# Performance work log

Hardware: AMD Instinct MI355X
Metric: run time of the kernel (lower is better)

## Reference

```python
import jax, jax.numpy as jnp
import numpy as np

B, T, D_IN, H, NUM_CLASSES = 512, 1024, 4, 64, 1098


def setup_inputs() -> dict:
    key = jax.random.key(0)
    ks = jax.random.split(key, 20)
    s = 1.0 / np.sqrt(H)  # PyTorch LSTM init range

    def w(k, shape):
        return jax.random.uniform(k, shape, jnp.float32, -s, s)

    inp = {}
    inp['x'] = jax.random.normal(ks[0], (B, T, D_IN), jnp.float32)
    lens = jax.random.randint(ks[1], (B,), 1, T + 1)
    inp['lengths'] = jnp.sort(lens)[::-1]  # descending, like pack_sequence
    i = 2
    for layer, d in ((0, D_IN), (1, 2 * H)):
        for dirn in ('f', 'b'):
            inp[f'W_ih_l{layer}{dirn}'] = w(ks[i], (4 * H, d)); i += 1
            inp[f'W_hh_l{layer}{dirn}'] = w(ks[i], (4 * H, H)); i += 1
            inp[f'b_ih_l{layer}{dirn}'] = w(ks[i], (4 * H,)); i += 1
            inp[f'b_hh_l{layer}{dirn}'] = w(ks[i], (4 * H,)); i += 1
    inp['W_out'] = w(ks[i], (NUM_CLASSES, 2 * H)); i += 1
    inp['b_out'] = w(ks[i], (NUM_CLASSES,))
    return inp


def _lstm_layer(x, W_ih, W_hh, b_ih, b_hh):
    # x: [B, T, D] -> outputs [B, T, H]; PyTorch gate order i, f, g, o
    Bb = x.shape[0]
    Hh = W_hh.shape[1]
    xW = jnp.einsum('btd,gd->btg', x, W_ih) + b_ih + b_hh  # [B, T, 4H]

    def step(carry, xt):
        h, c = carry
        g = xt + h @ W_hh.T
        i, f, gg, o = jnp.split(g, 4, axis=-1)
        c = jax.nn.sigmoid(f) * c + jax.nn.sigmoid(i) * jnp.tanh(gg)
        h = jax.nn.sigmoid(o) * jnp.tanh(c)
        return (h, c), h

    init = (jnp.zeros((Bb, Hh), x.dtype), jnp.zeros((Bb, Hh), x.dtype))
    _, hs = jax.lax.scan(step, init, jnp.swapaxes(xW, 0, 1))
    return jnp.swapaxes(hs, 0, 1)


def _reverse_padded(x, lengths):
    # per-sequence time reversal within the valid length (packed-seq semantics)
    Tt = x.shape[1]
    t = jnp.arange(Tt)
    idx = jnp.where(t[None, :] < lengths[:, None], lengths[:, None] - 1 - t[None, :], t[None, :])
    return jnp.take_along_axis(x, idx[:, :, None], axis=1)


def _bidir_layer(x, lengths, pf, pb):
    hf = _lstm_layer(x, *pf)
    hb = _reverse_padded(_lstm_layer(_reverse_padded(x, lengths), *pb), lengths)
    return jnp.concatenate([hf, hb], axis=-1)


def reference(x, lengths,
              W_ih_l0f, W_hh_l0f, b_ih_l0f, b_hh_l0f,
              W_ih_l0b, W_hh_l0b, b_ih_l0b, b_hh_l0b,
              W_ih_l1f, W_hh_l1f, b_ih_l1f, b_hh_l1f,
              W_ih_l1b, W_hh_l1b, b_ih_l1b, b_hh_l1b,
              W_out, b_out):
    h = _bidir_layer(x, lengths,
                     (W_ih_l0f, W_hh_l0f, b_ih_l0f, b_hh_l0f),
                     (W_ih_l0b, W_hh_l0b, b_ih_l0b, b_hh_l0b))
    h = _bidir_layer(h, lengths,
                     (W_ih_l1f, W_hh_l1f, b_ih_l1f, b_hh_l1f),
                     (W_ih_l1b, W_hh_l1b, b_ih_l1b, b_hh_l1b))
    # gather last valid timestep per sequence: [B, 2H]
    lasts = jnp.take_along_axis(h, (lengths - 1)[:, None, None], axis=1)[:, 0]
    return lasts @ W_out.T + b_out
```

## Files before the change

kernel.cpp:

```cpp
#include <hip/hip_runtime.h>
#include <stdint.h>

#define BATCH 512
#define TMAX  1024
#define DIN   4
#define H     64
#define NC    1098
#define RCH   32

typedef __attribute__((ext_vector_type(2))) float    v2;
typedef __attribute__((ext_vector_type(2))) _Float16 h2;

__device__ __forceinline__ v2 mkv2(float a, float b) { v2 r; r.x = a; r.y = b; return r; }
__device__ __forceinline__ float sigmoidf_(float x) { return 1.0f / (1.0f + __expf(-x)); }
__device__ __forceinline__ float tanhf_(float x) { return 1.0f - 2.0f / (__expf(2.0f * x) + 1.0f); }
__device__ __forceinline__ uint32_t f2bf(float f) {
    uint32_t u = __float_as_uint(f);
    return (u + 0x7FFFu + ((u >> 16) & 1u)) >> 16;
}
__device__ __forceinline__ float bf2f(uint32_t h) { return __uint_as_float(h << 16); }
__device__ __forceinline__ h2 u2h(uint32_t u) { union { uint32_t u; h2 h; } c; c.u = u; return c.h; }

__device__ __forceinline__ float fdot2_(h2 w, h2 x, float acc) {
    return __builtin_amdgcn_fdot2(w, x, acc, false);
}

__global__ __launch_bounds__(128) void lstm_l0(
    const float* __restrict__ x, const int* __restrict__ lengths,
    const float* __restrict__ Wih_f, const float* __restrict__ Whh_f,
    const float* __restrict__ bih_f, const float* __restrict__ bhh_f,
    const float* __restrict__ Wih_b, const float* __restrict__ Whh_b,
    const float* __restrict__ bih_b, const float* __restrict__ bhh_b,
    uint16_t* __restrict__ h0b )
{
    const int b = blockIdx.x;
    const int t = threadIdx.x;
    const int j = t & 63, dir = t >> 6;
    const int L = lengths[b];

    const float* Wih = dir ? Wih_b : Wih_f;
    const float* Whh = dir ? Whh_b : Whh_f;
    const float* bih = dir ? bih_b : bih_f;
    const float* bhh = dir ? bhh_b : bhh_f;

    h2 wh[4][32];
    #pragma unroll
    for (int g = 0; g < 4; g++) {
        const float4* pw = (const float4*)(Whh + (size_t)(64*g + j) * H);
        #pragma unroll
        for (int k = 0; k < 16; k++) {
            float4 a = pw[k];
            h2 lo; lo.x = (_Float16)a.x; lo.y = (_Float16)a.y;
            h2 hi; hi.x = (_Float16)a.z; hi.y = (_Float16)a.w;
            wh[g][2*k]   = lo;
            wh[g][2*k+1] = hi;
        }
    }
    float4 wx[4]; float bb[4];
    #pragma unroll
    for (int g = 0; g < 4; g++) {
        wx[g] = ((const float4*)Wih)[64*g + j];
        bb[g] = bih[64*g + j] + bhh[64*g + j];
    }

    __shared__ __align__(16) float4    xbuf[TMAX];
    __shared__ __align__(16) _Float16  hb16[2][H];
    {
        const float4* x4 = (const float4*)x + (size_t)b * TMAX;
        for (int i = t; i < L; i += 128) xbuf[i] = x4[i];
    }
    hb16[dir][j] = (_Float16)0.0f;
    float c = 0.0f;
    __syncthreads();

    uint16_t* outp = h0b + (size_t)b * TMAX * (2*H) + dir * H + j;

    for (int s = 0; s < L; s++) {
        const int tt = dir ? (L - 1 - s) : s;
        const float4 xt = xbuf[tt];
        float p[4];
        #pragma unroll
        for (int g = 0; g < 4; g++)
            p[g] = fmaf(wx[g].w, xt.w, fmaf(wx[g].z, xt.z,
                   fmaf(wx[g].y, xt.y, fmaf(wx[g].x, xt.x, bb[g]))));
        float acA[4] = {0.f,0.f,0.f,0.f}, acB[4] = {0.f,0.f,0.f,0.f};
        const uint4* h4 = (const uint4*)&hb16[dir][0];
        #pragma unroll
        for (int q = 0; q < 8; q++) {
            uint4 u = h4[q];
            h2 p0 = u2h(u.x), p1 = u2h(u.y), p2 = u2h(u.z), p3 = u2h(u.w);
            #pragma unroll
            for (int g = 0; g < 4; g++) {
                acA[g] = fdot2_(wh[g][4*q+0], p0, acA[g]);
                acA[g] = fdot2_(wh[g][4*q+1], p1, acA[g]);
                acB[g] = fdot2_(wh[g][4*q+2], p2, acB[g]);
                acB[g] = fdot2_(wh[g][4*q+3], p3, acB[g]);
            }
        }
        #pragma unroll
        for (int g = 0; g < 4; g++) p[g] += acA[g] + acB[g];
        const float gi = sigmoidf_(p[0]);
        const float gf = sigmoidf_(p[1]);
        const float gg = tanhf_(p[2]);
        const float go = sigmoidf_(p[3]);
        c = fmaf(gf, c, gi * gg);
        const float h = go * tanhf_(c);
        hb16[dir][j] = (_Float16)h;
        outp[(size_t)tt * (2*H)] = (uint16_t)f2bf(h);
    }
}

__global__ __launch_bounds__(512) void lstm_rec_pipe(
    const uint16_t* __restrict__ h0b, const int* __restrict__ lengths,
    const float* __restrict__ Wih, const float* __restrict__ Whh,
    const float* __restrict__ bih, const float* __restrict__ bhh,
    const float* __restrict__ Wih_b,
    const float* __restrict__ bih_b, const float* __restrict__ bhh_b,
    const float* __restrict__ Wout, const float* __restrict__ bout,
    float* __restrict__ out)
{
    const int b = blockIdx.x;
    const int t = threadIdx.x;
    const int j = t & 63, w = t >> 6;
    const int L = lengths[b];
    const bool isProd = (w < 4);

    __shared__ __align__(16) float xch[RCH * 128];
    __shared__ __align__(16) float part[2][4][256];
    __shared__ __align__(16) float hrep[4][H];
    __shared__ __align__(16) float ex[2][4][H];
    __shared__ __align__(16) float ybuf[2*H];

    v2 wreg[64];
    float bias = 0.0f;
    if (isProd) {
        #pragma unroll
        for (int q = 0; q < 4; q++) {
            const float4* pw = (const float4*)(Wih + (size_t)(4*j + q) * 128 + 32 * w);
            #pragma unroll
            for (int k = 0; k < 8; k++) {
                float4 v = pw[k];
                wreg[q*16 + 2*k]     = mkv2(v.x, v.y);
                wreg[q*16 + 2*k + 1] = mkv2(v.z, v.w);
            }
        }
    } else {
        const int g = (w - 4) * H + j;
        const float4* pw = (const float4*)(Whh + (size_t)g * H);
        #pragma unroll
        for (int k = 0; k < 16; k++) {
            float4 v = pw[k];
            wreg[2*k]     = mkv2(v.x, v.y);
            wreg[2*k + 1] = mkv2(v.z, v.w);
        }
        bias = bih[g] + bhh[g];
        hrep[w - 4][j] = 0.0f;
    }
    float c = 0.0f, h = 0.0f;

    auto produce = [&](int r, int p) {
        const float4* xr = (const float4*)(xch + r * 128 + 32 * w);
        v2 a0 = mkv2(0,0), a1 = mkv2(0,0), a2 = mkv2(0,0), a3 = mkv2(0,0);
        #pragma unroll
        for (int k = 0; k < 8; k++) {
            float4 xv = xr[k];
            v2 xlo = mkv2(xv.x, xv.y), xhi = mkv2(xv.z, xv.w);
            a0 += wreg[ 0 + 2*k] * xlo; a0 += wreg[ 0 + 2*k + 1] * xhi;
            a1 += wreg[16 + 2*k] * xlo; a1 += wreg[16 + 2*k + 1] * xhi;
            a2 += wreg[32 + 2*k] * xlo; a2 += wreg[32 + 2*k + 1] * xhi;
            a3 += wreg[48 + 2*k] * xlo; a3 += wreg[48 + 2*k + 1] * xhi;
        }
        *(float4*)&part[p][w][4*j] =
            make_float4(a0.x + a0.y, a1.x + a1.y, a2.x + a2.y, a3.x + a3.y);
    };

    for (int s = 0; s < L; s++) {
        const int rr = s & (RCH - 1);
        if (rr == 0) {
            __syncthreads();
            const uint32_t* src = (const uint32_t*)(h0b + ((size_t)b * TMAX + s) * (2*H));
            for (int i = t; i < RCH * 64; i += 512) {
                uint32_t u = src[i];
                *(float2*)(xch + 2*i) = make_float2(bf2f(u & 0xFFFFu), bf2f(u >> 16));
            }
            __syncthreads();
            if (isProd) produce(0, s & 1);
            __syncthreads();
        }
        if (isProd) {
            if (s + 1 < L && rr + 1 < RCH)
                produce(rr + 1, (s + 1) & 1);
        } else {
            const int g = (w - 4) * H + j;
            const float pa = part[s & 1][0][g] + part[s & 1][1][g]
                           + part[s & 1][2][g] + part[s & 1][3][g];
            v2 a0 = mkv2(pa + bias, 0.0f), a1 = mkv2(0.0f, 0.0f);
            const float4* h4 = (const float4*)hrep[w - 4];
            #pragma unroll
            for (int k = 0; k < 16; k++) {
                float4 hv = h4[k];
                a0 += wreg[2*k]     * mkv2(hv.x, hv.y);
                a1 += wreg[2*k + 1] * mkv2(hv.z, hv.w);
            }
            const float a = (a0.x + a0.y) + (a1.x + a1.y);
            ex[s & 1][w - 4][j] = (w == 6) ? tanhf_(a) : sigmoidf_(a);
        }
        __syncthreads();
        if (!isProd) {
            const int p = s & 1;
            const float gi = ex[p][0][j], gf = ex[p][1][j];
            const float gg = ex[p][2][j], go = ex[p][3][j];
            c = fmaf(gf, c, gi * gg);
            h = go * tanhf_(c);
            hrep[w - 4][j] = h;
        }
    }

    if (w == 4) ybuf[j] = h;
    __syncthreads();
    const float* xrow = xch + ((L - 1) & (RCH - 1)) * 128;
    float* gb = &part[0][0][0];
    if (t < 256) {
        const float4* wb = (const float4*)(Wih_b + (size_t)t * 128);
        const float4* xv = (const float4*)xrow;
        v2 a0 = mkv2(bih_b[t] + bhh_b[t], 0.0f), a1 = mkv2(0.0f, 0.0f);
        #pragma unroll
        for (int k = 0; k < 32; k++) {
            float4 wv = wb[k], xk = xv[k];
            a0 += mkv2(wv.x, wv.y) * mkv2(xk.x, xk.y);
            a1 += mkv2(wv.z, wv.w) * mkv2(xk.z, xk.w);
        }
        const float a = (a0.x + a0.y) + (a1.x + a1.y);
        gb[t] = (t >= 128 && t < 192) ? tanhf_(a) : sigmoidf_(a);
    }
    __syncthreads();
    if (t < 64) {
        const float gi = gb[t], gg = gb[128 + t], go = gb[192 + t];
        ybuf[H + t] = go * tanhf_(gi * gg);
    }
    __syncthreads();

    const float4* yv = (const float4*)ybuf;
    for (int o = t; o < NC; o += 512) {
        const float4* wr = (const float4*)(Wout + (size_t)o * (2*H));
        v2 a0 = mkv2(bout[o], 0.0f), a1 = mkv2(0.0f, 0.0f);
        #pragma unroll
        for (int k = 0; k < 32; k++) {
            float4 wv = wr[k], yy = yv[k];
            a0 += mkv2(wv.x, wv.y) * mkv2(yy.x, yy.y);
            a1 += mkv2(wv.z, wv.w) * mkv2(yy.z, yy.w);
        }
        out[(size_t)b * NC + o] = (a0.x + a0.y) + (a1.x + a1.y);
    }
}

extern "C" void kernel_launch(void* const* d_in, const int* in_sizes, int n_in,
                              void* d_out, int out_size, void* d_ws, size_t ws_size,
                              hipStream_t stream) {
    const float* x        = (const float*)d_in[0];
    const int*   lengths  = (const int*)  d_in[1];
    const float* Wih_l0f  = (const float*)d_in[2];
    const float* Whh_l0f  = (const float*)d_in[3];
    const float* bih_l0f  = (const float*)d_in[4];
    const float* bhh_l0f  = (const float*)d_in[5];
    const float* Wih_l0b  = (const float*)d_in[6];
    const float* Whh_l0b  = (const float*)d_in[7];
    const float* bih_l0b  = (const float*)d_in[8];
    const float* bhh_l0b  = (const float*)d_in[9];
    const float* Wih_l1f  = (const float*)d_in[10];
    const float* Whh_l1f  = (const float*)d_in[11];
    const float* bih_l1f  = (const float*)d_in[12];
    const float* bhh_l1f  = (const float*)d_in[13];
    const float* Wih_l1b  = (const float*)d_in[14];
    const float* bih_l1b  = (const float*)d_in[16];
    const float* bhh_l1b  = (const float*)d_in[17];
    const float* Wout     = (const float*)d_in[18];
    const float* bout     = (const float*)d_in[19];
    float* out = (float*)d_out;

    uint16_t* h0b = (uint16_t*)d_ws;

    lstm_l0<<<dim3(BATCH), 128, 0, stream>>>(
        x, lengths,
        Wih_l0f, Whh_l0f, bih_l0f, bhh_l0f,
        Wih_l0b, Whh_l0b, bih_l0b, bhh_l0b, h0b);

    lstm_rec_pipe<<<dim3(BATCH), 512, 0, stream>>>(
        h0b, lengths,
        Wih_l1f, Whh_l1f, bih_l1f, bhh_l1f,
        Wih_l1b, bih_l1b, bhh_l1b, Wout, bout, out);
}
```

Before: 1.340 ms.

## Pair long and short sequences per block and restructure layer-1 recurrence pipeline

Each block of both kernels now processes two sequences, index bk and BATCH-1-bk, to balance the sorted lengths across blocks. The grid is halved. Layer 1 is rebuilt so a single wave per sequence runs the recurrence using fp16 dot2 weights in registers. Two producer waves compute the input projection in fp16 for chunks of 8 timesteps, double-buffering the staged h0 rows. The intermediate h0 moves from bf16 to fp16. This cuts the per-step block barriers and the idle time caused by uneven lengths, at the cost of lower input-projection precision and fewer threads per sequence.

```diff
diff --git a/kernel.cpp b/kernel.cpp
--- a/kernel.cpp
+++ b/kernel.cpp
@@ -3,10 +3,9 @@
 
 #define BATCH 512
 #define TMAX  1024
-#define DIN   4
+#define NC    1098
 #define H     64
-#define NC    1098
-#define RCH   32
+#define CH    8
 
 typedef __attribute__((ext_vector_type(2))) float    v2;
 typedef __attribute__((ext_vector_type(2))) _Float16 h2;
@@ -14,29 +13,27 @@
 __device__ __forceinline__ v2 mkv2(float a, float b) { v2 r; r.x = a; r.y = b; return r; }
 __device__ __forceinline__ float sigmoidf_(float x) { return 1.0f / (1.0f + __expf(-x)); }
 __device__ __forceinline__ float tanhf_(float x) { return 1.0f - 2.0f / (__expf(2.0f * x) + 1.0f); }
-__device__ __forceinline__ uint32_t f2bf(float f) {
-    uint32_t u = __float_as_uint(f);
-    return (u + 0x7FFFu + ((u >> 16) & 1u)) >> 16;
-}
-__device__ __forceinline__ float bf2f(uint32_t h) { return __uint_as_float(h << 16); }
 __device__ __forceinline__ h2 u2h(uint32_t u) { union { uint32_t u; h2 h; } c; c.u = u; return c.h; }
 
 __device__ __forceinline__ float fdot2_(h2 w, h2 x, float acc) {
     return __builtin_amdgcn_fdot2(w, x, acc, false);
 }
 
-__global__ __launch_bounds__(128) void lstm_l0(
+__global__ __launch_bounds__(256) void lstm_l0(
     const float* __restrict__ x, const int* __restrict__ lengths,
     const float* __restrict__ Wih_f, const float* __restrict__ Whh_f,
     const float* __restrict__ bih_f, const float* __restrict__ bhh_f,
     const float* __restrict__ Wih_b, const float* __restrict__ Whh_b,
     const float* __restrict__ bih_b, const float* __restrict__ bhh_b,
-    uint16_t* __restrict__ h0b )
+    _Float16* __restrict__ h0 )
 {
-    const int b = blockIdx.x;
+    const int bk = blockIdx.x;
     const int t = threadIdx.x;
-    const int j = t & 63, dir = t >> 6;
-    const int L = lengths[b];
+    const int j = t & 63, w = t >> 6;
+    const int seq = (w < 2) ? bk : (BATCH - 1 - bk);
+    const int dir = w & 1;
+    const int xb  = w >> 1;
+    const int L = lengths[seq];
 
     const float* Wih = dir ? Wih_b : Wih_f;
     const float* Whh = dir ? Whh_b : Whh_f;
@@ -63,28 +60,32 @@
         bb[g] = bih[64*g + j] + bhh[64*g + j];
     }
 
-    __shared__ __align__(16) float4    xbuf[TMAX];
-    __shared__ __align__(16) _Float16  hb16[2][H];
+    __shared__ __align__(16) float4    xbuf[2][TMAX];
+    __shared__ __align__(16) _Float16  hln[4][H];
     {
-        const float4* x4 = (const float4*)x + (size_t)b * TMAX;
-        for (int i = t; i < L; i += 128) xbuf[i] = x4[i];
-    }
-    hb16[dir][j] = (_Float16)0.0f;
+        const int sA = bk, sB = BATCH - 1 - bk;
+        const int LA = lengths[sA], LB = lengths[sB];
+        const float4* xA = (const float4*)x + (size_t)sA * TMAX;
+        const float4* xB = (const float4*)x + (size_t)sB * TMAX;
+        for (int i = t; i < LA; i += 256) xbuf[0][i] = xA[i];
+        for (int i = t; i < LB; i += 256) xbuf[1][i] = xB[i];
+    }
+    hln[w][j] = (_Float16)0.0f;
     float c = 0.0f;
     __syncthreads();
 
-    uint16_t* outp = h0b + (size_t)b * TMAX * (2*H) + dir * H + j;
+    _Float16* outp = h0 + (size_t)seq * TMAX * 128 + dir * H + j;
 
     for (int s = 0; s < L; s++) {
         const int tt = dir ? (L - 1 - s) : s;
-        const float4 xt = xbuf[tt];
+        const float4 xt = xbuf[xb][tt];
         float p[4];
         #pragma unroll
         for (int g = 0; g < 4; g++)
             p[g] = fmaf(wx[g].w, xt.w, fmaf(wx[g].z, xt.z,
                    fmaf(wx[g].y, xt.y, fmaf(wx[g].x, xt.x, bb[g]))));
         float acA[4] = {0.f,0.f,0.f,0.f}, acB[4] = {0.f,0.f,0.f,0.f};
-        const uint4* h4 = (const uint4*)&hb16[dir][0];
+        const uint4* h4 = (const uint4*)&hln[w][0];
         #pragma unroll
         for (int q = 0; q < 8; q++) {
             uint4 u = h4[q];
@@ -105,152 +106,193 @@
         const float go = sigmoidf_(p[3]);
         c = fmaf(gf, c, gi * gg);
         const float h = go * tanhf_(c);
-        hb16[dir][j] = (_Float16)h;
-        outp[(size_t)tt * (2*H)] = (uint16_t)f2bf(h);
+        hln[w][j] = (_Float16)h;
+        outp[(size_t)tt * 128] = (_Float16)h;
     }
 }
 
-__global__ __launch_bounds__(512) void lstm_rec_pipe(
-    const uint16_t* __restrict__ h0b, const int* __restrict__ lengths,
-    const float* __restrict__ Wih, const float* __restrict__ Whh,
-    const float* __restrict__ bih, const float* __restrict__ bhh,
-    const float* __restrict__ Wih_b,
-    const float* __restrict__ bih_b, const float* __restrict__ bhh_b,
+__global__ __launch_bounds__(384) void lstm_l1(
+    const _Float16* __restrict__ h0, const int* __restrict__ lengths,
+    const float* __restrict__ Wih,  const float* __restrict__ Whh,
+    const float* __restrict__ bih,  const float* __restrict__ bhh,
+    const float* __restrict__ WihB, const float* __restrict__ bihB,
+    const float* __restrict__ bhhB,
     const float* __restrict__ Wout, const float* __restrict__ bout,
     float* __restrict__ out)
 {
-    const int b = blockIdx.x;
+    const int bk = blockIdx.x;
     const int t = threadIdx.x;
-    const int j = t & 63, w = t >> 6;
-    const int L = lengths[b];
-    const bool isProd = (w < 4);
-
-    __shared__ __align__(16) float xch[RCH * 128];
-    __shared__ __align__(16) float part[2][4][256];
-    __shared__ __align__(16) float hrep[4][H];
-    __shared__ __align__(16) float ex[2][4][H];
-    __shared__ __align__(16) float ybuf[2*H];
-
-    v2 wreg[64];
-    float bias = 0.0f;
-    if (isProd) {
-        #pragma unroll
-        for (int q = 0; q < 4; q++) {
-            const float4* pw = (const float4*)(Wih + (size_t)(4*j + q) * 128 + 32 * w);
-            #pragma unroll
-            for (int k = 0; k < 8; k++) {
-                float4 v = pw[k];
-                wreg[q*16 + 2*k]     = mkv2(v.x, v.y);
-                wreg[q*16 + 2*k + 1] = mkv2(v.z, v.w);
-            }
-        }
-    } else {
-        const int g = (w - 4) * H + j;
-        const float4* pw = (const float4*)(Whh + (size_t)g * H);
-        #pragma unroll
-        for (int k = 0; k < 16; k++) {
-            float4 v = pw[k];
-            wreg[2*k]     = mkv2(v.x, v.y);
-            wreg[2*k + 1] = mkv2(v.z, v.w);
-        }
-        bias = bih[g] + bhh[g];
-        hrep[w - 4][j] = 0.0f;
-    }
-    float c = 0.0f, h = 0.0f;
-
-    auto produce = [&](int r, int p) {
-        const float4* xr = (const float4*)(xch + r * 128 + 32 * w);
-        v2 a0 = mkv2(0,0), a1 = mkv2(0,0), a2 = mkv2(0,0), a3 = mkv2(0,0);
-        #pragma unroll
-        for (int k = 0; k < 8; k++) {
-            float4 xv = xr[k];
-            v2 xlo = mkv2(xv.x, xv.y), xhi = mkv2(xv.z, xv.w);
-            a0 += wreg[ 0 + 2*k] * xlo; a0 += wreg[ 0 + 2*k + 1] * xhi;
-            a1 += wreg[16 + 2*k] * xlo; a1 += wreg[16 + 2*k + 1] * xhi;
-            a2 += wreg[32 + 2*k] * xlo; a2 += wreg[32 + 2*k + 1] * xhi;
-            a3 += wreg[48 + 2*k] * xlo; a3 += wreg[48 + 2*k + 1] * xhi;
-        }
-        *(float4*)&part[p][w][4*j] =
-            make_float4(a0.x + a0.y, a1.x + a1.y, a2.x + a2.y, a3.x + a3.y);
-    };
-
-    for (int s = 0; s < L; s++) {
-        const int rr = s & (RCH - 1);
-        if (rr == 0) {
-            __syncthreads();
-            const uint32_t* src = (const uint32_t*)(h0b + ((size_t)b * TMAX + s) * (2*H));
-            for (int i = t; i < RCH * 64; i += 512) {
-                uint32_t u = src[i];
-                *(float2*)(xch + 2*i) = make_float2(bf2f(u & 0xFFFFu), bf2f(u >> 16));
-            }
-            __syncthreads();
-            if (isProd) produce(0, s & 1);
-            __syncthreads();
-        }
-        if (isProd) {
-            if (s + 1 < L && rr + 1 < RCH)
-                produce(rr + 1, (s + 1) & 1);
-        } else {
-            const int g = (w - 4) * H + j;
-            const float pa = part[s & 1][0][g] + part[s & 1][1][g]
-                           + part[s & 1][2][g] + part[s & 1][3][g];
-            v2 a0 = mkv2(pa + bias, 0.0f), a1 = mkv2(0.0f, 0.0f);
-            const float4* h4 = (const float4*)hrep[w - 4];
+    const int grp = (t >= 192) ? 1 : 0;
+    const int tl = t - 192 * grp;
+    const int wl = tl >> 6;
+    const int l = tl & 63;
+    const int seq = grp ? (BATCH - 1 - bk) : bk;
+    const int L = lengths[seq];
+    const int nch = (L + CH - 1) / CH;
+    const int nchMax = (lengths[bk] + CH - 1) / CH;
+
+    __shared__ __align__(16) float    xw[2][2][CH][256];
+    __shared__ __align__(16) _Float16 hst[2][2][CH][128];
+    __shared__ __align__(16) _Float16 hln[2][H];
+    __shared__ __align__(16) float    ybuf[2][2*H];
+    __shared__ __align__(16) float    gb[2][192];
+    __shared__ __align__(16) float    h0r[2][128];
+
+    const _Float16* hseq = h0 + (size_t)seq * TMAX * 128;
+
+    h2 wsh[128];
+    float bb[4] = {0.f, 0.f, 0.f, 0.f};
+    int rA = 0, rB = 0;
+    if (wl == 0) {
+        #pragma unroll
+        for (int g = 0; g < 4; g++) {
+            const float4* pw = (const float4*)(Whh + (size_t)(64*g + l) * H);
             #pragma unroll
             for (int k = 0; k < 16; k++) {
-                float4 hv = h4[k];
-                a0 += wreg[2*k]     * mkv2(hv.x, hv.y);
-                a1 += wreg[2*k + 1] * mkv2(hv.z, hv.w);
+                float4 a = pw[k];
+                h2 lo; lo.x = (_Float16)a.x; lo.y = (_Float16)a.y;
+                h2 hi; hi.x = (_Float16)a.z; hi.y = (_Float16)a.w;
+                wsh[g*32 + 2*k]   = lo;
+                wsh[g*32 + 2*k+1] = hi;
             }
-            const float a = (a0.x + a0.y) + (a1.x + a1.y);
-            ex[s & 1][w - 4][j] = (w == 6) ? tanhf_(a) : sigmoidf_(a);
+            bb[g] = bih[64*g + l] + bhh[64*g + l];
+        }
+        hln[grp][l] = (_Float16)0.0f;
+    } else {
+        const int pw = wl - 1;
+        rA = pw * 128 + l; rB = pw * 128 + 64 + l;
+        const float4* pa = (const float4*)(Wih + (size_t)rA * 128);
+        const float4* pb = (const float4*)(Wih + (size_t)rB * 128);
+        #pragma unroll
+        for (int k = 0; k < 32; k++) {
+            float4 a = pa[k], b2 = pb[k];
+            h2 alo; alo.x = (_Float16)a.x;  alo.y = (_Float16)a.y;
+            h2 ahi; ahi.x = (_Float16)a.z;  ahi.y = (_Float16)a.w;
+            h2 blo; blo.x = (_Float16)b2.x; blo.y = (_Float16)b2.y;
+            h2 bhi; bhi.x = (_Float16)b2.z; bhi.y = (_Float16)b2.w;
+            wsh[2*k]        = alo;
+            wsh[2*k + 1]    = ahi;
+            wsh[64 + 2*k]   = blo;
+            wsh[64 + 2*k+1] = bhi;
+        }
+    }
+
+    uint4 st0;
+    auto stage_load = [&](int ck) {
+        const uint4* gp = (const uint4*)(hseq + (size_t)ck * CH * 128);
+        st0 = gp[(wl - 1) * 64 + l];
+    };
+    auto stage_store = [&](int ck) {
+        uint4* dp = (uint4*)&hst[grp][ck & 1][0][0];
+        dp[(wl - 1) * 64 + l] = st0;
+    };
+    auto produce = [&](int ck) {
+        const int par = ck & 1;
+        for (int r = 0; r < CH; r++) {
+            const uint4* rp = (const uint4*)&hst[grp][par][r][0];
+            float aA = 0.f, aB = 0.f;
+            #pragma unroll
+            for (int q = 0; q < 16; q++) {
+                uint4 u = rp[q];
+                h2 p0 = u2h(u.x), p1 = u2h(u.y), p2 = u2h(u.z), p3 = u2h(u.w);
+                aA = fdot2_(wsh[4*q+0], p0, aA);
+                aA = fdot2_(wsh[4*q+1], p1, aA);
+                aA = fdot2_(wsh[4*q+2], p2, aA);
+                aA = fdot2_(wsh[4*q+3], p3, aA);
+                aB = fdot2_(wsh[64+4*q+0], p0, aB);
+                aB = fdot2_(wsh[64+4*q+1], p1, aB);
+                aB = fdot2_(wsh[64+4*q+2], p2, aB);
+                aB = fdot2_(wsh[64+4*q+3], p3, aB);
+            }
+            xw[grp][par][r][rA] = aA;
+            xw[grp][par][r][rB] = aB;
+        }
+    };
+
+    float c = 0.f, h = 0.f;
+
+    if (wl >= 1) { stage_load(0); stage_store(0); if (nch > 1) stage_load(1); }
+    __syncthreads();
+    if (wl >= 1) { produce(0); if (nch > 1) stage_store(1); }
+    __syncthreads();
+
+    for (int cc = 0; cc < nchMax; cc++) {
+        if (wl == 0) {
+            const int sbeg = cc * CH;
+            const int send = (sbeg + CH < L) ? (sbeg + CH) : L;
+            const int par = cc & 1;
+            for (int s = sbeg; s < send; s++) {
+                const int r = s - sbeg;
+                float p[4];
+                #pragma unroll
+                for (int g = 0; g < 4; g++)
+                    p[g] = xw[grp][par][r][g*64 + l] + bb[g];
+                float acA[4] = {0.f,0.f,0.f,0.f}, acB[4] = {0.f,0.f,0.f,0.f};
+                const uint4* h4 = (const uint4*)&hln[grp][0];
+                #pragma unroll
+                for (int q = 0; q < 8; q++) {
+                    uint4 u = h4[q];
+                    h2 p0 = u2h(u.x), p1 = u2h(u.y), p2 = u2h(u.z), p3 = u2h(u.w);
+                    #pragma unroll
+                    for (int g = 0; g < 4; g++) {
+                        acA[g] = fdot2_(wsh[g*32+4*q+0], p0, acA[g]);
+                        acA[g] = fdot2_(wsh[g*32+4*q+1], p1, acA[g]);
+                        acB[g] = fdot2_(wsh[g*32+4*q+2], p2, acB[g]);
+                        acB[g] = fdot2_(wsh[g*32+4*q+3], p3, acB[g]);
+                    }
+                }
+                #pragma unroll
+                for (int g = 0; g < 4; g++) p[g] += acA[g] + acB[g];
+                const float gi = sigmoidf_(p[0]);
+                const float gf = sigmoidf_(p[1]);
+                const float gg = tanhf_(p[2]);
+                const float go = sigmoidf_(p[3]);
+                c = fmaf(gf, c, gi * gg);
+                h = go * tanhf_(c);
+                hln[grp][l] = (_Float16)h;
+            }
+        } else {
+            if (cc + 2 < nch) stage_load(cc + 2);
+            if (cc + 1 < nch) produce(cc + 1);
+            if (cc + 2 < nch) stage_store(cc + 2);
         }
         __syncthreads();
-        if (!isProd) {
-            const int p = s & 1;
-            const float gi = ex[p][0][j], gf = ex[p][1][j];
-            const float gg = ex[p][2][j], go = ex[p][3][j];
-            c = fmaf(gf, c, gi * gg);
-            h = go * tanhf_(c);
-            hrep[w - 4][j] = h;
-        }
-    }
-
-    if (w == 4) ybuf[j] = h;
-    __syncthreads();
-    const float* xrow = xch + ((L - 1) & (RCH - 1)) * 128;
-    float* gb = &part[0][0][0];
-    if (t < 256) {
-        const float4* wb = (const float4*)(Wih_b + (size_t)t * 128);
-        const float4* xv = (const float4*)xrow;
-        v2 a0 = mkv2(bih_b[t] + bhh_b[t], 0.0f), a1 = mkv2(0.0f, 0.0f);
+    }
+
+    if (wl == 0) ybuf[grp][l] = h;
+    if (tl < 128) h0r[grp][tl] = (float)hseq[(size_t)(L - 1) * 128 + tl];
+    __syncthreads();
+    {
+        const int row = (tl < 64) ? tl : (tl + 64);
+        const float4* wr = (const float4*)(WihB + (size_t)row * 128);
+        const float4* xr = (const float4*)&h0r[grp][0];
+        v2 a0 = mkv2(bihB[row] + bhhB[row], 0.f), a1 = mkv2(0.f, 0.f);
         #pragma unroll
         for (int k = 0; k < 32; k++) {
-            float4 wv = wb[k], xk = xv[k];
-            a0 += mkv2(wv.x, wv.y) * mkv2(xk.x, xk.y);
-            a1 += mkv2(wv.z, wv.w) * mkv2(xk.z, xk.w);
+            float4 wv = wr[k], xv = xr[k];
+            a0 += mkv2(wv.x, wv.y) * mkv2(xv.x, xv.y);
+            a1 += mkv2(wv.z, wv.w) * mkv2(xv.z, xv.w);
         }
         const float a = (a0.x + a0.y) + (a1.x + a1.y);
-        gb[t] = (t >= 128 && t < 192) ? tanhf_(a) : sigmoidf_(a);
-    }
-    __syncthreads();
-    if (t < 64) {
-        const float gi = gb[t], gg = gb[128 + t], go = gb[192 + t];
-        ybuf[H + t] = go * tanhf_(gi * gg);
-    }
-    __syncthreads();
-
-    const float4* yv = (const float4*)ybuf;
-    for (int o = t; o < NC; o += 512) {
-        const float4* wr = (const float4*)(Wout + (size_t)o * (2*H));
-        v2 a0 = mkv2(bout[o], 0.0f), a1 = mkv2(0.0f, 0.0f);
+        gb[grp][tl] = (tl >= 64 && tl < 128) ? tanhf_(a) : sigmoidf_(a);
+    }
+    __syncthreads();
+    if (tl < 64) {
+        const float hb = gb[grp][128 + tl] * tanhf_(gb[grp][tl] * gb[grp][64 + tl]);
+        ybuf[grp][H + tl] = hb;
+    }
+    __syncthreads();
+    const float4* yv = (const float4*)&ybuf[grp][0];
+    for (int o = tl; o < NC; o += 192) {
+        const float4* wr = (const float4*)(Wout + (size_t)o * 128);
+        v2 a0 = mkv2(bout[o], 0.f), a1 = mkv2(0.f, 0.f);
         #pragma unroll
         for (int k = 0; k < 32; k++) {
             float4 wv = wr[k], yy = yv[k];
             a0 += mkv2(wv.x, wv.y) * mkv2(yy.x, yy.y);
             a1 += mkv2(wv.z, wv.w) * mkv2(yy.z, yy.w);
         }
-        out[(size_t)b * NC + o] = (a0.x + a0.y) + (a1.x + a1.y);
+        out[(size_t)seq * NC + o] = (a0.x + a0.y) + (a1.x + a1.y);
     }
 }
 
@@ -278,15 +320,15 @@
     const float* bout     = (const float*)d_in[19];
     float* out = (float*)d_out;
 
-    uint16_t* h0b = (uint16_t*)d_ws;
-
-    lstm_l0<<<dim3(BATCH), 128, 0, stream>>>(
+    _Float16* h0 = (_Float16*)d_ws;
+
+    lstm_l0<<<dim3(BATCH / 2), 256, 0, stream>>>(
         x, lengths,
         Wih_l0f, Whh_l0f, bih_l0f, bhh_l0f,
-        Wih_l0b, Whh_l0b, bih_l0b, bhh_l0b, h0b);
-
-    lstm_rec_pipe<<<dim3(BATCH), 512, 0, stream>>>(
-        h0b, lengths,
+        Wih_l0b, Whh_l0b, bih_l0b, bhh_l0b, h0);
+
+    lstm_l1<<<dim3(BATCH / 2), 384, 0, stream>>>(
+        h0, lengths,
         Wih_l1f, Whh_l1f, bih_l1f, bhh_l1f,
         Wih_l1b, bih_l1b, bhh_l1b, Wout, bout, out);
 }
```

New measurement: 1.212 ms. 1.11x faster.
